# Performance work log

Measured on AMD Instinct MI355X. Metric: run time of the kernel, lower is better.

Reference implementation:

```python
import jax, jax.numpy as jnp
import numpy as np

OUT_FEATURES = 4096
IN_FEATURES = 4096
GROUP_SIZE = 16


def setup_inputs() -> dict:
    key = jax.random.key(0)
    k1, k2, k3, k4 = jax.random.split(key, 4)
    n_groups = OUT_FEATURES * IN_FEATURES // GROUP_SIZE
    x = jax.random.normal(k1, (8, 2048, IN_FEATURES), dtype=jnp.float32)
    weight_q = jax.random.randint(k2, (n_groups, GROUP_SIZE), 0, 16, dtype=jnp.int32).astype(jnp.int8)
    weight_norm = jax.random.uniform(k3, (n_groups, 1), dtype=jnp.float32).astype(jnp.float16)
    bias = jax.random.normal(k4, (OUT_FEATURES,), dtype=jnp.float32)
    return {"x": x, "weight_q": weight_q, "weight_norm": weight_norm, "bias": bias}


def reference(x, weight_q, weight_norm, bias):
    # block dequant: (q/15) * per-group scale, then reshape to [out, in]
    w = (weight_q.astype(jnp.float32) / 15.0) * weight_norm.astype(jnp.float32)
    w = w.reshape(OUT_FEATURES, IN_FEATURES)
    # F.linear: x @ w^T + bias
    return jnp.einsum('bsi,oi->bso', x, w) + bias
```

## Files before the change

### kernel.cpp

```cpp
#include <hip/hip_runtime.h>

#define MDIM 16384
#define NDIM 4096
#define KDIM 4096
#define NT   64

typedef unsigned short u16;
typedef unsigned int   u32;
typedef __attribute__((ext_vector_type(8))) short bh8;
typedef __attribute__((ext_vector_type(4))) float f32x4;
typedef __attribute__((ext_vector_type(16))) float f32x16;
typedef __attribute__((ext_vector_type(4))) int   i32x4;

__device__ __forceinline__ u16 f2bf(float f) {
  u32 u = __builtin_bit_cast(u32, f);
  u = (u + 0x7fffu + ((u >> 16) & 1u)) >> 16;
  return (u16)u;
}

__device__ __forceinline__ void gld16(const void* g, const void* lds) {
  __builtin_amdgcn_global_load_lds((const __attribute__((address_space(1))) u32*)g,
                                   (__attribute__((address_space(3))) u32*)lds, 16, 0, 0);
}

__global__ void cvt_x(const float* __restrict__ x, u16* __restrict__ xb) {
  size_t i = ((size_t)blockIdx.x * 256 + threadIdx.x) * 8;
  f32x4 a = *(const f32x4*)(x + i);
  f32x4 b = *(const f32x4*)(x + i + 4);
  bh8 o;
  o[0] = (short)f2bf(a[0]); o[1] = (short)f2bf(a[1]);
  o[2] = (short)f2bf(a[2]); o[3] = (short)f2bf(a[3]);
  o[4] = (short)f2bf(b[0]); o[5] = (short)f2bf(b[1]);
  o[6] = (short)f2bf(b[2]); o[7] = (short)f2bf(b[3]);
  *(bh8*)(xb + i) = o;
}

__global__ void deq_w(const int* __restrict__ qi, const void* __restrict__ nrm,
                      u16* __restrict__ wb) {
  __shared__ int s_q8, s_n32;
  if (threadIdx.x == 0) {
    int packed = 0;
    for (int t = 0; t < 64; ++t) { unsigned v = (unsigned)qi[t]; if (v > 15u) packed = 1; }
    int n32 = 0;
    const u16* h = (const u16*)nrm;
    for (int t = 0; t < 64; ++t) { u16 b = h[t]; if (b < 0x8000u && b > 0x3C00u) n32 = 1; }
    s_q8 = packed; s_n32 = n32;
  }
  __syncthreads();
  const bool q8 = (s_q8 != 0), n32 = (s_n32 != 0);

  int g = blockIdx.x * 256 + threadIdx.x;
  float s;
  if (n32) s = ((const float*)nrm)[g] * (1.0f / 15.0f);
  else {
    u16 hb = ((const u16*)nrm)[g];
    s = (float)__builtin_bit_cast(_Float16, hb) * (1.0f / 15.0f);
  }
  float q[16];
  if (q8) {
    i32x4 v = *(const i32x4*)((const unsigned char*)qi + (size_t)g * 16);
#pragma unroll
    for (int k = 0; k < 4; ++k) {
      int word = v[k];
      q[k*4+0] = (float)(word & 255);        q[k*4+1] = (float)((word >> 8) & 255);
      q[k*4+2] = (float)((word >> 16) & 255); q[k*4+3] = (float)((word >> 24) & 255);
    }
  } else {
    const i32x4* p = (const i32x4*)(qi + (size_t)g * 16);
#pragma unroll
    for (int k = 0; k < 4; ++k) {
      i32x4 v = p[k];
      q[k*4+0] = (float)v[0]; q[k*4+1] = (float)v[1];
      q[k*4+2] = (float)v[2]; q[k*4+3] = (float)v[3];
    }
  }
  bh8 o0, o1;
#pragma unroll
  for (int j = 0; j < 8; ++j) o0[j] = (short)f2bf(q[j] * s);
#pragma unroll
  for (int j = 0; j < 8; ++j) o1[j] = (short)f2bf(q[8 + j] * s);
  *(bh8*)(wb + (size_t)g * 16) = o0;
  *(bh8*)(wb + (size_t)g * 16 + 8) = o1;
}

__global__ __launch_bounds__(512, 2) void gemm8(const u16* __restrict__ A,
                                                const u16* __restrict__ B,
                                                const float* __restrict__ bias,
                                                float* __restrict__ out) {
  __shared__ u16 lds[65536];
  const int tid = threadIdx.x;
  const int w = tid >> 6, l = tid & 63;
  const int wm = w >> 2, wn = w & 3;

  int bid = blockIdx.x;
  int wg = (bid & 7) * 128 + (bid >> 3);
  const int bm = wg >> 4;
  const int bn = wg & 15;

  const u16* aSrcF = A + (size_t)(bm * 256 + (l & 31)) * 4096 + (l >> 5) * 8;
  const u16* bSrcF = B + (size_t)(bn * 256 + (l & 31)) * 4096 + (l >> 5) * 8;

  f32x16 acc[4][2];
#pragma unroll
  for (int mi = 0; mi < 4; ++mi)
#pragma unroll
    for (int ni = 0; ni < 2; ++ni)
#pragma unroll
      for (int r = 0; r < 16; ++r) acc[mi][ni][r] = 0.f;

  bh8 aX[4], aY[4];
  bh8 bf_[2][4];

  auto STG = [&](int op, int h, int t) {
    const int f0 = h * 16 + w * 2;
    const int mb = f0 >> 2, s = f0 & 3;
    const u16* src = (op ? bSrcF : aSrcF) + mb * 131072 + s * 16 + t * 64;
    const int d = (op ? 32768 : 0) + (t & 1) * 16384 + f0 * 512;
    gld16(src,      &lds[d]);
    gld16(src + 16, &lds[d + 512]);
  };
  auto RDA = [&](int buf, int mbl, bh8 (&aa)[4]) {
    const int base = buf * 16384 + (wm * 4 + mbl) * 2048 + l * 8;
#pragma unroll
    for (int s = 0; s < 4; ++s) aa[s] = *(const bh8*)&lds[base + s * 512];
  };
  auto RDB = [&](int buf) {
#pragma unroll
    for (int nbl = 0; nbl < 2; ++nbl) {
      const int base = 32768 + buf * 16384 + (wn * 2 + nbl) * 2048 + l * 8;
#pragma unroll
      for (int s = 0; s < 4; ++s) bf_[nbl][s] = *(const bh8*)&lds[base + s * 512];
    }
  };
  auto MMB = [&](int mbl, bh8 (&aa)[4]) {
    __builtin_amdgcn_s_setprio(1);
#pragma unroll
    for (int s = 0; s < 4; ++s)
#pragma unroll
      for (int nbl = 0; nbl < 2; ++nbl)
        acc[mbl][nbl] = __builtin_amdgcn_mfma_f32_32x32x16_bf16(
            aa[s], bf_[nbl][s], acc[mbl][nbl], 0, 0, 0);
    __builtin_amdgcn_s_setprio(0);
  };

#define BAR1 asm volatile("" ::: "memory"); __builtin_amdgcn_s_barrier(); \
             asm volatile("" ::: "memory");
#define BAR2 asm volatile("" ::: "memory"); __builtin_amdgcn_s_barrier();

  STG(1, 0, 0); STG(1, 1, 0); STG(0, 0, 0); STG(0, 1, 0);
  STG(1, 0, 1); STG(1, 1, 1); STG(0, 0, 1); STG(0, 1, 1);
  asm volatile("s_waitcnt vmcnt(8)");
  BAR1;
  RDA(0, 0, aX);

#pragma unroll 1
  for (int i = 0; i < NT / 2 - 1; ++i) {
    const int c = 2 * i + 2, d = 2 * i + 3;
    RDB(0); RDA(0, 1, aY);
    BAR1; MMB(0, aX); BAR2;
    RDA(0, 2, aX); STG(1, 0, c);
    BAR1; MMB(1, aY); BAR2;
    RDA(0, 3, aY); STG(1, 1, c);
    BAR1; MMB(2, aX); BAR2;
    STG(0, 0, c); asm volatile("s_waitcnt vmcnt(6)");
    BAR1; RDA(1, 0, aX); MMB(3, aY); BAR2;
    RDB(1); RDA(1, 1, aY); STG(0, 1, c);
    BAR1; MMB(0, aX); BAR2;
    RDA(1, 2, aX); STG(1, 0, d);
    BAR1; MMB(1, aY); BAR2;
    RDA(1, 3, aY); STG(1, 1, d);
    BAR1; MMB(2, aX); BAR2;
    STG(0, 0, d); STG(0, 1, d); asm volatile("s_waitcnt vmcnt(8)");
    BAR1; RDA(0, 0, aX); MMB(3, aY); BAR2;
  }
  RDB(0); RDA(0, 1, aY);
  BAR1; MMB(0, aX); BAR2;
  RDA(0, 2, aX);
  BAR1; MMB(1, aY); BAR2;
  RDA(0, 3, aY);
  BAR1; MMB(2, aX); BAR2;
  asm volatile("s_waitcnt vmcnt(0)");
  BAR1; RDA(1, 0, aX); MMB(3, aY); BAR2;
  RDB(1); RDA(1, 1, aY);
  BAR1; MMB(0, aX); BAR2;
  RDA(1, 2, aX);
  BAR1; MMB(1, aY); BAR2;
  RDA(1, 3, aY);
  BAR1; MMB(2, aX); BAR2;
  BAR1; MMB(3, aY);
#undef BAR1
#undef BAR2

  const int colb = bn * 256 + wn * 64 + (l & 31);
  const int rowb = bm * 256 + wm * 128 + 4 * (l >> 5);
#pragma unroll
  for (int nbl = 0; nbl < 2; ++nbl) {
    float bv = bias[colb + nbl * 32];
#pragma unroll
    for (int mbl = 0; mbl < 4; ++mbl) {
#pragma unroll
      for (int r = 0; r < 16; ++r) {
        int row = rowb + mbl * 32 + (r & 3) + 8 * (r >> 2);
        out[(size_t)row * 4096 + colb + nbl * 32] = acc[mbl][nbl][r] + bv;
      }
    }
  }
}

__global__ __launch_bounds__(512, 2) void gemm_fb(const float* __restrict__ Af32,
                                                  const u16* __restrict__ Wbf,
                                                  const float* __restrict__ bias,
                                                  float* __restrict__ out) {
  __shared__ u16 lds[65536];
  const int tid = threadIdx.x;
  const int w = tid >> 6, l = tid & 63;
  const int wm = w >> 2, wn = w & 3;
  int bid = blockIdx.x;
  int wg = (bid & 7) * 128 + (bid >> 3);
  const int bm = wg >> 4, bn = wg & 15;

  int srcOffB[4], srcOffA32[4], dstSwzA[4];
#pragma unroll
  for (int j = 0; j < 4; ++j) {
    int ci = (w * 4 + j) * 64 + l;
    int r = ci >> 3, c = ci & 7;
    int cs = c ^ (r & 7);
    srcOffB[j]   = (bn * 256 + r) * 4096 + cs * 8;
    srcOffA32[j] = (bm * 256 + r) * 4096 + c * 8;
    dstSwzA[j]   = r * 64 + cs * 8;
  }
  const int ar = wm * 128 + (l & 15);
  const int br = wn * 64 + (l & 15);
  const int swz0 = (((l >> 4) + 0) ^ (l & 7)) * 8;
  const int swz1 = (((l >> 4) + 4) ^ (l & 7)) * 8;
  const int aoff0 = ar * 64 + swz0, aoff1 = ar * 64 + swz1;
  const int boff0 = 32768 + br * 64 + swz0, boff1 = 32768 + br * 64 + swz1;

  f32x4 acc[8][4];
#pragma unroll
  for (int mi = 0; mi < 8; ++mi)
#pragma unroll
    for (int ni = 0; ni < 4; ++ni) acc[mi][ni] = (f32x4){0.f, 0.f, 0.f, 0.f};

  auto STAGE = [&](int bufb, int kt) {
    const int kof = kt * 64;
#pragma unroll
    for (int j = 0; j < 4; ++j) {
      gld16(Wbf + srcOffB[j] + kof, &lds[32768 + bufb * 16384 + (w * 4 + j) * 512]);
      const float* p = Af32 + srcOffA32[j] + kof;
      f32x4 v0 = *(const f32x4*)p;
      f32x4 v1 = *(const f32x4*)(p + 4);
      bh8 o;
      o[0] = (short)f2bf(v0[0]); o[1] = (short)f2bf(v0[1]);
      o[2] = (short)f2bf(v0[2]); o[3] = (short)f2bf(v0[3]);
      o[4] = (short)f2bf(v1[0]); o[5] = (short)f2bf(v1[1]);
      o[6] = (short)f2bf(v1[2]); o[7] = (short)f2bf(v1[3]);
      *(bh8*)&lds[bufb * 16384 + dstSwzA[j]] = o;
    }
  };
  auto COMPUTE = [&](int bufb) {
    const int ab = bufb * 16384;
#pragma unroll
    for (int kk = 0; kk < 2; ++kk) {
      const int ao = ab + (kk ? aoff1 : aoff0);
      const int bo = ab + (kk ? boff1 : boff0);
      bh8 afr[8], bfr[4];
#pragma unroll
      for (int mi = 0; mi < 8; ++mi) afr[mi] = *(const bh8*)&lds[ao + mi * 1024];
#pragma unroll
      for (int ni = 0; ni < 4; ++ni) bfr[ni] = *(const bh8*)&lds[bo + ni * 1024];
#pragma unroll
      for (int mi = 0; mi < 8; ++mi)
#pragma unroll
        for (int ni = 0; ni < 4; ++ni)
          acc[mi][ni] = __builtin_amdgcn_mfma_f32_16x16x32_bf16(afr[mi], bfr[ni],
                                                                acc[mi][ni], 0, 0, 0);
    }
  };

  int buf = 0;
  STAGE(0, 0);
  __syncthreads();
  for (int kt = 0; kt < NT - 1; ++kt) {
    STAGE(buf ^ 1, kt + 1);
    COMPUTE(buf);
    __syncthreads();
    buf ^= 1;
  }
  COMPUTE(buf);

  const int col0 = bn * 256 + wn * 64 + (l & 15);
  const int row0 = bm * 256 + wm * 128 + (l >> 4) * 4;
#pragma unroll
  for (int ni = 0; ni < 4; ++ni) {
    float bv = bias[col0 + ni * 16];
#pragma unroll
    for (int mi = 0; mi < 8; ++mi) {
      size_t base = (size_t)(row0 + mi * 16) * 4096 + (size_t)(col0 + ni * 16);
#pragma unroll
      for (int rr = 0; rr < 4; ++rr)
        out[base + (size_t)rr * 4096] = acc[mi][ni][rr] + bv;
    }
  }
}

extern "C" void kernel_launch(void* const* d_in, const int* in_sizes, int n_in,
                              void* d_out, int out_size, void* d_ws, size_t ws_size,
                              hipStream_t stream) {
  const float* x    = (const float*)d_in[0];
  const int*   wq   = (const int*)d_in[1];
  const void*  wn   = d_in[2];
  const float* bias = (const float*)d_in[3];
  float*       out  = (float*)d_out;

  const size_t needA = (size_t)MDIM * KDIM * 2;
  const size_t needW = (size_t)NDIM * KDIM * 2;

  if (ws_size >= needA + needW) {
    u16* xbf = (u16*)d_ws;
    u16* wbf = (u16*)((char*)d_ws + needA);
    cvt_x<<<dim3(32768), dim3(256), 0, stream>>>(x, xbf);
    deq_w<<<dim3(4096), dim3(256), 0, stream>>>(wq, wn, wbf);
    gemm8<<<dim3(1024), dim3(512), 0, stream>>>(xbf, wbf, bias, out);
  } else if (ws_size >= needW) {
    u16* wbf = (u16*)d_ws;
    deq_w<<<dim3(4096), dim3(256), 0, stream>>>(wq, wn, wbf);
    gemm_fb<<<dim3(1024), dim3(512), 0, stream>>>(x, wbf, bias, out);
  }
}
```

Baseline: 659.6 us.

## Use row-major XOR-swizzled LDS layout for global-to-LDS tile loads

Changes how the bf16 A and B tiles are staged through global_load_lds. Each wave now loads whole 128-byte row segments with an XOR swizzle on the 16-byte chunk index. The MFMA fragment reads apply the matching swizzle. The goal is more contiguous global accesses per wave and fewer LDS bank conflicts on the fragment reads, at the cost of extra per-lane index arithmetic.

```diff
diff --git a/kernel.cpp b/kernel.cpp
--- a/kernel.cpp
+++ b/kernel.cpp
@@ -97,8 +97,14 @@
   const int bm = wg >> 4;
   const int bn = wg & 15;
 
-  const u16* aSrcF = A + (size_t)(bm * 256 + (l & 31)) * 4096 + (l >> 5) * 8;
-  const u16* bSrcF = B + (size_t)(bn * 256 + (l & 31)) * 4096 + (l >> 5) * 8;
+  const int cs8  = ((l & 7) ^ (l >> 3)) * 8;
+  const u16* aSrc = A + (size_t)(bm * 256 + w * 32 + (l >> 3)) * 4096 + cs8;
+  const u16* bSrc = B + (size_t)(bn * 256 + w * 32 + (l >> 3)) * 4096 + cs8;
+
+  const int hreg = (l >> 4) & 1;
+  const int rloc = (l & 15) * 64;
+  const int x7   = l & 7;
+  const int chi  = l >> 5;
 
   f32x16 acc[4][2];
 #pragma unroll
@@ -111,25 +117,25 @@
   bh8 aX[4], aY[4];
   bh8 bf_[2][4];
 
-  auto STG = [&](int op, int h, int t) {
-    const int f0 = h * 16 + w * 2;
-    const int mb = f0 >> 2, s = f0 & 3;
-    const u16* src = (op ? bSrcF : aSrcF) + mb * 131072 + s * 16 + t * 64;
-    const int d = (op ? 32768 : 0) + (t & 1) * 16384 + f0 * 512;
-    gld16(src,      &lds[d]);
-    gld16(src + 16, &lds[d + 512]);
-  };
-  auto RDA = [&](int buf, int mbl, bh8 (&aa)[4]) {
-    const int base = buf * 16384 + (wm * 4 + mbl) * 2048 + l * 8;
-#pragma unroll
-    for (int s = 0; s < 4; ++s) aa[s] = *(const bh8*)&lds[base + s * 512];
+  auto STG = [&](int op, int h, int kt) {
+    const u16* s = (op ? bSrc : aSrc) + h * 65536 + kt * 64;
+    int d = (op ? 32768 : 0) + ((kt & 1) * 2 + h) * 8192 + w * 1024;
+    gld16(s,         &lds[d]);
+    gld16(s + 32768, &lds[d + 512]);
+  };
+  auto RDA = [&](int buf, int mb, bh8 (&aa)[4]) {
+    const int base = (buf * 2 + hreg) * 8192 + (wm * 4 + mb) * 1024 + rloc;
+#pragma unroll
+    for (int s = 0; s < 4; ++s)
+      aa[s] = *(const bh8*)&lds[base + ((s * 2 + chi) ^ x7) * 8];
   };
   auto RDB = [&](int buf) {
 #pragma unroll
-    for (int nbl = 0; nbl < 2; ++nbl) {
-      const int base = 32768 + buf * 16384 + (wn * 2 + nbl) * 2048 + l * 8;
-#pragma unroll
-      for (int s = 0; s < 4; ++s) bf_[nbl][s] = *(const bh8*)&lds[base + s * 512];
+    for (int nb = 0; nb < 2; ++nb) {
+      const int base = 32768 + (buf * 2 + hreg) * 8192 + (wn * 2 + nb) * 1024 + rloc;
+#pragma unroll
+      for (int s = 0; s < 4; ++s)
+        bf_[nb][s] = *(const bh8*)&lds[base + ((s * 2 + chi) ^ x7) * 8];
     }
   };
   auto MMB = [&](int mbl, bh8 (&aa)[4]) {
@@ -137,9 +143,9 @@
 #pragma unroll
     for (int s = 0; s < 4; ++s)
 #pragma unroll
-      for (int nbl = 0; nbl < 2; ++nbl)
-        acc[mbl][nbl] = __builtin_amdgcn_mfma_f32_32x32x16_bf16(
-            aa[s], bf_[nbl][s], acc[mbl][nbl], 0, 0, 0);
+      for (int nb = 0; nb < 2; ++nb)
+        acc[mbl][nb] = __builtin_amdgcn_mfma_f32_32x32x16_bf16(
+            aa[s], bf_[nb][s], acc[mbl][nb], 0, 0, 0);
     __builtin_amdgcn_s_setprio(0);
   };
 
@@ -194,14 +200,14 @@
   const int colb = bn * 256 + wn * 64 + (l & 31);
   const int rowb = bm * 256 + wm * 128 + 4 * (l >> 5);
 #pragma unroll
-  for (int nbl = 0; nbl < 2; ++nbl) {
-    float bv = bias[colb + nbl * 32];
+  for (int nb = 0; nb < 2; ++nb) {
+    float bv = bias[colb + nb * 32];
 #pragma unroll
     for (int mbl = 0; mbl < 4; ++mbl) {
 #pragma unroll
       for (int r = 0; r < 16; ++r) {
         int row = rowb + mbl * 32 + (r & 3) + 8 * (r >> 2);
-        out[(size_t)row * 4096 + colb + nbl * 32] = acc[mbl][nbl][r] + bv;
+        out[(size_t)row * 4096 + colb + nb * 32] = acc[mbl][nb][r] + bv;
       }
     }
   }
```

Result: faster. 588.9 us (-10.7%).
